# Kernel tuning notes

Measured on AMD Instinct MI355X. Metric: run time of the kernel, lower is better.

Reference implementation:

```python
import jax, jax.numpy as jnp
import numpy as np

N_NODES = 100000
N_EDGES = 1000000
D_FEAT = 64


def setup_inputs() -> dict:
    key = jax.random.key(0)
    k1, k2 = jax.random.split(key)
    x = jax.random.normal(k1, (N_NODES, D_FEAT), dtype=jnp.float32)
    edge_index = jax.random.randint(k2, (2, N_EDGES), 0, N_NODES, dtype=jnp.int64)
    return {"x": x, "edge_index": edge_index}


def reference(x, edge_index):
    # message: x_j = x[edge_index[1]]  (per-edge gather)
    # aggregate: scatter_add into destination nodes edge_index[0], dim_size = N
    # update: identity
    msg = x[edge_index[1]]                                  # [E, d]
    out = jax.ops.segment_sum(msg, edge_index[0], num_segments=x.shape[0])  # [N, d]
    return out
```

## Files before the change

### kernel.cpp

```cpp
#include <hip/hip_runtime.h>

#define D_FEAT     64
#define CSHIFT     8
#define CNODES     256
#define MAXC       512
#define CCAP       3072
#define CNT_STRIDE 16
#define PACK_SHIFT 24
#define PSRC_MASK  ((1 << PACK_SHIFT) - 1)
#define P_BLOCK    512
#define P_EPT      8
#define PB_EDGES   (P_BLOCK * P_EPT)
#define A_BLOCK    512
#define QCAP       1024

__global__ __launch_bounds__(256) void mp_scatter_kernel(
    const float* __restrict__ x,
    const int* __restrict__ ei,
    float* __restrict__ out,
    int E) {
    long long tid = (long long)blockIdx.x * blockDim.x + threadIdx.x;
    int e = (int)(tid >> 6);
    int f = (int)(tid & 63);
    if (e >= E) return;
    int dst = ei[e];
    int src = ei[E + e];
    float v = x[(long long)src * D_FEAT + f];
    unsafeAtomicAdd(&out[(long long)dst * D_FEAT + f], v);
}

__global__ __launch_bounds__(P_BLOCK) void partition_edges(
    const int* __restrict__ ei, int E, int nbins,
    int* __restrict__ binCount,
    int* __restrict__ binList) {
    __shared__ int  hist[MAXC];
    __shared__ int  loff[MAXC];
    __shared__ int  gbase[MAXC];
    __shared__ int  cur[MAXC];
    __shared__ int2 sOut[PB_EDGES];

    int t = threadIdx.x;
    for (int b = t; b < nbins; b += P_BLOCK) hist[b] = 0;
    __syncthreads();

    int start = blockIdx.x * PB_EDGES;
    int ecnt = E - start; if (ecnt > PB_EDGES) ecnt = PB_EDGES;

#pragma unroll
    for (int k = 0; k < P_EPT; ++k) {
        int i = k * P_BLOCK + t;
        if (i < ecnt) atomicAdd(&hist[ei[start + i] >> CSHIFT], 1);
    }
    __syncthreads();

    if (t < 64) {
        int chunk = (nbins + 63) >> 6;
        int base_i = t * chunk;
        int vals[8];
        int sum = 0;
        for (int k = 0; k < chunk; ++k) {
            int b = base_i + k;
            vals[k] = (b < nbins) ? hist[b] : 0;
            sum += vals[k];
        }
        int inc = sum;
#pragma unroll
        for (int d = 1; d < 64; d <<= 1) {
            int y = __shfl_up(inc, d, 64);
            if (t >= d) inc += y;
        }
        int excl = inc - sum;
        for (int k = 0; k < chunk; ++k) {
            int b = base_i + k;
            if (b < nbins) { loff[b] = excl; cur[b] = excl; excl += vals[k]; }
        }
    }
    __syncthreads();

    for (int b = t; b < nbins; b += P_BLOCK) {
        int h = hist[b];
        if (h) gbase[b] = atomicAdd(&binCount[b * CNT_STRIDE], h);
    }
    __syncthreads();

#pragma unroll
    for (int k = 0; k < P_EPT; ++k) {
        int i = k * P_BLOCK + t;
        if (i < ecnt) {
            int dst = ei[start + i];
            int src = ei[E + start + i];
            int b = dst >> CSHIFT;
            int r = atomicAdd(&cur[b], 1);
            int gpos = gbase[b] + (r - loff[b]);
            int slot = (gpos < CCAP) ? (b * CCAP + gpos) : -1;
            sOut[r] = make_int2(slot,
                                (int)(((unsigned)(dst & (CNODES - 1)) << PACK_SHIFT) |
                                      (unsigned)src));
        }
    }
    __syncthreads();

    for (int i = t; i < ecnt; i += P_BLOCK) {
        int2 o = sOut[i];
        if (o.x >= 0) binList[o.x] = o.y;
    }
}

__global__ __launch_bounds__(A_BLOCK, 8) void bin_accumulate(
    const float* __restrict__ x,
    const int* __restrict__ binCount,
    const int* __restrict__ binList,
    float* __restrict__ out,
    int N) {
    __shared__ int sList[CCAP];
    __shared__ int sCsr[QCAP];
    __shared__ int sCnt[64];
    __shared__ int sOff[64];
    __shared__ int sRank[64];

    int coarse  = blockIdx.x >> 2;
    int quarter = blockIdx.x & 3;
    int t = threadIdx.x;

    int cnt = binCount[coarse * CNT_STRIDE];
    if (cnt > CCAP) cnt = CCAP;

    if (t < 64) sCnt[t] = 0;
    __syncthreads();

    for (int i = t; i < cnt; i += A_BLOCK) {
        int p = binList[coarse * CCAP + i];
        sList[i] = p;
        unsigned ld = ((unsigned)p) >> PACK_SHIFT;
        if ((int)(ld >> 6) == quarter) atomicAdd(&sCnt[ld & 63], 1);
    }
    __syncthreads();

    if (t < 64) {
        int c = sCnt[t];
        int inc = c;
#pragma unroll
        for (int d = 1; d < 64; d <<= 1) {
            int y = __shfl_up(inc, d, 64);
            if (t >= d) inc += y;
        }
        sOff[t] = inc - c;
        sRank[t] = inc - c;
    }
    __syncthreads();

    for (int i = t; i < cnt; i += A_BLOCK) {
        int p = sList[i];
        unsigned ld = ((unsigned)p) >> PACK_SHIFT;
        if ((int)(ld >> 6) == quarter) {
            int r = atomicAdd(&sRank[ld & 63], 1);
            if (r < QCAP) sCsr[r] = p & PSRC_MASK;
        }
    }
    __syncthreads();

    int wave = t >> 6;
    int lane = t & 63;
    int q    = lane >> 4;
    int sub  = lane & 15;

    int nodeBase = (coarse << CSHIFT) + (quarter << 6);
    int nodesInQ = N - nodeBase; if (nodesInQ > 64) nodesInQ = 64;

    for (int n = wave; n < nodesInQ; n += 8) {
        int off = sOff[n];
        int deg = sCnt[n];
        if (off + deg > QCAP) deg = (QCAP > off) ? (QCAP - off) : 0;
        float4 acc = make_float4(0.f, 0.f, 0.f, 0.f);

        for (int e0 = 0; e0 < deg; e0 += 16) {
            float4 v[4];
#pragma unroll
            for (int j = 0; j < 4; ++j) {
                int eidx = e0 + j * 4 + q;
                v[j] = make_float4(0.f, 0.f, 0.f, 0.f);
                if (eidx < deg) {
                    int s = sCsr[off + eidx];
                    v[j] = ((const float4*)(x + (long long)s * D_FEAT))[sub];
                }
            }
#pragma unroll
            for (int j = 0; j < 4; ++j) {
                acc.x += v[j].x; acc.y += v[j].y;
                acc.z += v[j].z; acc.w += v[j].w;
            }
        }

        acc.x += __shfl_xor(acc.x, 16, 64);
        acc.y += __shfl_xor(acc.y, 16, 64);
        acc.z += __shfl_xor(acc.z, 16, 64);
        acc.w += __shfl_xor(acc.w, 16, 64);
        acc.x += __shfl_xor(acc.x, 32, 64);
        acc.y += __shfl_xor(acc.y, 32, 64);
        acc.z += __shfl_xor(acc.z, 32, 64);
        acc.w += __shfl_xor(acc.w, 32, 64);

        if (q == 0) {
            float4* out4 = (float4*)(out + (long long)(nodeBase + n) * D_FEAT);
            out4[sub] = acc;
        }
    }
}

extern "C" void kernel_launch(void* const* d_in, const int* in_sizes, int n_in,
                              void* d_out, int out_size, void* d_ws, size_t ws_size,
                              hipStream_t stream) {
    const float* x   = (const float*)d_in[0];
    const int*   ei  = (const int*)d_in[1];
    float*       out = (float*)d_out;

    int E = in_sizes[1] / 2;
    int N = out_size / D_FEAT;
    int nbins = (N + CNODES - 1) >> CSHIFT;

    size_t list_bytes  = (size_t)nbins * CCAP * sizeof(int);
    size_t count_bytes = (size_t)nbins * CNT_STRIDE * sizeof(int);
    size_t need = list_bytes + count_bytes;

    if (nbins > MAXC || N > (1 << PACK_SHIFT) || ws_size < need) {
        hipMemsetAsync(out, 0, (size_t)out_size * sizeof(float), stream);
        long long total = (long long)E * D_FEAT;
        int block = 256;
        int grid = (int)((total + block - 1) / block);
        mp_scatter_kernel<<<grid, block, 0, stream>>>(x, ei, out, E);
        return;
    }

    int* binList  = (int*)d_ws;
    int* binCount = (int*)((char*)d_ws + list_bytes);

    hipMemsetAsync(binCount, 0, count_bytes, stream);

    {
        int grid = (E + PB_EDGES - 1) / PB_EDGES;
        partition_edges<<<grid, P_BLOCK, 0, stream>>>(ei, E, nbins, binCount, binList);
    }
    {
        bin_accumulate<<<nbins * 4, A_BLOCK, 0, stream>>>(x, binCount, binList, out, N);
    }
}
```

Baseline: 128.0 us.

## Vectorize edge loads, halve accumulate blocks, and process two nodes per wave

The partition kernel now loads four contiguous edges per thread as int4 into registers, with half the edges per block, so the index array is read once instead of twice. The accumulate kernel splits each coarse bin into halves of 128 nodes instead of quarters of 64, which cuts the redundant rereads of binList per bin. It copies the bin list with int4 loads and has each wave interleave the gathers for two nodes so more loads are in flight. The cost is more registers, a lower occupancy hint, and work wasted when the two interleaved nodes have unequal degrees.

```diff
diff --git a/kernel.cpp b/kernel.cpp
--- a/kernel.cpp
+++ b/kernel.cpp
@@ -9,10 +9,10 @@
 #define PACK_SHIFT 24
 #define PSRC_MASK  ((1 << PACK_SHIFT) - 1)
 #define P_BLOCK    512
-#define P_EPT      8
+#define P_EPT      4
 #define PB_EDGES   (P_BLOCK * P_EPT)
 #define A_BLOCK    512
-#define QCAP       1024
+#define HCAP       2048
 
 __global__ __launch_bounds__(256) void mp_scatter_kernel(
     const float* __restrict__ x,
@@ -41,15 +41,31 @@
 
     int t = threadIdx.x;
     for (int b = t; b < nbins; b += P_BLOCK) hist[b] = 0;
-    __syncthreads();
 
     int start = blockIdx.x * PB_EDGES;
     int ecnt = E - start; if (ecnt > PB_EDGES) ecnt = PB_EDGES;
 
+    int dk[P_EPT], sk[P_EPT];
+    bool vec = (ecnt == PB_EDGES) && ((E & 3) == 0);
+    if (vec) {
+        int4 d4 = ((const int4*)(ei + start))[t];
+        int4 s4 = ((const int4*)(ei + E + start))[t];
+        dk[0] = d4.x; dk[1] = d4.y; dk[2] = d4.z; dk[3] = d4.w;
+        sk[0] = s4.x; sk[1] = s4.y; sk[2] = s4.z; sk[3] = s4.w;
+    } else {
+#pragma unroll
+        for (int k = 0; k < P_EPT; ++k) {
+            int i = t * P_EPT + k;
+            dk[k] = (i < ecnt) ? ei[start + i] : 0;
+            sk[k] = (i < ecnt) ? ei[E + start + i] : 0;
+        }
+    }
+    __syncthreads();
+
 #pragma unroll
     for (int k = 0; k < P_EPT; ++k) {
-        int i = k * P_BLOCK + t;
-        if (i < ecnt) atomicAdd(&hist[ei[start + i] >> CSHIFT], 1);
+        int i = t * P_EPT + k;
+        if (i < ecnt) atomicAdd(&hist[dk[k] >> CSHIFT], 1);
     }
     __syncthreads();
 
@@ -85,17 +101,16 @@
 
 #pragma unroll
     for (int k = 0; k < P_EPT; ++k) {
-        int i = k * P_BLOCK + t;
+        int i = t * P_EPT + k;
         if (i < ecnt) {
-            int dst = ei[start + i];
-            int src = ei[E + start + i];
+            int dst = dk[k];
             int b = dst >> CSHIFT;
             int r = atomicAdd(&cur[b], 1);
             int gpos = gbase[b] + (r - loff[b]);
             int slot = (gpos < CCAP) ? (b * CCAP + gpos) : -1;
             sOut[r] = make_int2(slot,
                                 (int)(((unsigned)(dst & (CNODES - 1)) << PACK_SHIFT) |
-                                      (unsigned)src));
+                                      (unsigned)sk[k]));
         }
     }
     __syncthreads();
@@ -106,55 +121,67 @@
     }
 }
 
-__global__ __launch_bounds__(A_BLOCK, 8) void bin_accumulate(
+__global__ __launch_bounds__(A_BLOCK, 6) void bin_accumulate(
     const float* __restrict__ x,
     const int* __restrict__ binCount,
     const int* __restrict__ binList,
     float* __restrict__ out,
     int N) {
     __shared__ int sList[CCAP];
-    __shared__ int sCsr[QCAP];
-    __shared__ int sCnt[64];
-    __shared__ int sOff[64];
-    __shared__ int sRank[64];
-
-    int coarse  = blockIdx.x >> 2;
-    int quarter = blockIdx.x & 3;
+    __shared__ int sCsr[HCAP];
+    __shared__ int sCnt[128];
+    __shared__ int sOff[128];
+    __shared__ int sRank[128];
+
+    int coarse = blockIdx.x >> 1;
+    int half   = blockIdx.x & 1;
     int t = threadIdx.x;
 
     int cnt = binCount[coarse * CNT_STRIDE];
     if (cnt > CCAP) cnt = CCAP;
 
-    if (t < 64) sCnt[t] = 0;
-    __syncthreads();
-
-    for (int i = t; i < cnt; i += A_BLOCK) {
-        int p = binList[coarse * CCAP + i];
-        sList[i] = p;
-        unsigned ld = ((unsigned)p) >> PACK_SHIFT;
-        if ((int)(ld >> 6) == quarter) atomicAdd(&sCnt[ld & 63], 1);
+    if (t < 128) sCnt[t] = 0;
+    __syncthreads();
+
+    const int4* bl4 = (const int4*)(binList + coarse * CCAP);
+    int nvec = (cnt + 3) >> 2;
+    for (int v = t; v < nvec; v += A_BLOCK) {
+        int4 e4 = bl4[v];
+        ((int4*)sList)[v] = e4;
+        int pk[4] = {e4.x, e4.y, e4.z, e4.w};
+        int i = v << 2;
+#pragma unroll
+        for (int j = 0; j < 4; ++j) {
+            if (i + j < cnt) {
+                unsigned ld = ((unsigned)pk[j]) >> PACK_SHIFT;
+                if ((int)(ld >> 7) == half) atomicAdd(&sCnt[ld & 127], 1);
+            }
+        }
     }
     __syncthreads();
 
     if (t < 64) {
-        int c = sCnt[t];
-        int inc = c;
+        int c0 = sCnt[2 * t];
+        int c1 = sCnt[2 * t + 1];
+        int sum = c0 + c1;
+        int inc = sum;
 #pragma unroll
         for (int d = 1; d < 64; d <<= 1) {
             int y = __shfl_up(inc, d, 64);
             if (t >= d) inc += y;
         }
-        sOff[t] = inc - c;
-        sRank[t] = inc - c;
+        int excl = inc - sum;
+        sOff[2 * t]     = excl;      sRank[2 * t]     = excl;
+        sOff[2 * t + 1] = excl + c0; sRank[2 * t + 1] = excl + c0;
     }
     __syncthreads();
 
     for (int i = t; i < cnt; i += A_BLOCK) {
         int p = sList[i];
         unsigned ld = ((unsigned)p) >> PACK_SHIFT;
-        if ((int)(ld >> 6) == quarter) {
-            int r = atomicAdd(&sRank[ld & 63], 1);
-            if (r < QCAP) sCsr[r] = p & PSRC_MASK;
+        if ((int)(ld >> 7) == half) {
+            int r = atomicAdd(&sRank[ld & 127], 1);
+            if (r < HCAP) sCsr[r] = p & PSRC_MASK;
         }
     }
     __syncthreads();
@@ -164,45 +191,78 @@
     int q    = lane >> 4;
     int sub  = lane & 15;
 
-    int nodeBase = (coarse << CSHIFT) + (quarter << 6);
-    int nodesInQ = N - nodeBase; if (nodesInQ > 64) nodesInQ = 64;
-
-    for (int n = wave; n < nodesInQ; n += 8) {
-        int off = sOff[n];
-        int deg = sCnt[n];
-        if (off + deg > QCAP) deg = (QCAP > off) ? (QCAP - off) : 0;
-        float4 acc = make_float4(0.f, 0.f, 0.f, 0.f);
-
-        for (int e0 = 0; e0 < deg; e0 += 16) {
-            float4 v[4];
+    int nodeBase = (coarse << CSHIFT) + (half << 7);
+    int nodesInH = N - nodeBase; if (nodesInH > 128) nodesInH = 128;
+
+    for (int n0 = wave; n0 < nodesInH; n0 += 16) {
+        int n1 = n0 + 8;
+        int hasB = (n1 < nodesInH);
+
+        int offA = sOff[n0];
+        int degA = sCnt[n0];
+        if (offA + degA > HCAP) degA = (HCAP > offA) ? (HCAP - offA) : 0;
+        int offB = 0, degB = 0;
+        if (hasB) {
+            offB = sOff[n1];
+            degB = sCnt[n1];
+            if (offB + degB > HCAP) degB = (HCAP > offB) ? (HCAP - offB) : 0;
+        }
+
+        float4 accA = make_float4(0.f, 0.f, 0.f, 0.f);
+        float4 accB = make_float4(0.f, 0.f, 0.f, 0.f);
+        int dmax = degA > degB ? degA : degB;
+
+        for (int e0 = 0; e0 < dmax; e0 += 16) {
+            float4 vA[4], vB[4];
 #pragma unroll
             for (int j = 0; j < 4; ++j) {
                 int eidx = e0 + j * 4 + q;
-                v[j] = make_float4(0.f, 0.f, 0.f, 0.f);
-                if (eidx < deg) {
-                    int s = sCsr[off + eidx];
-                    v[j] = ((const float4*)(x + (long long)s * D_FEAT))[sub];
+                vA[j] = make_float4(0.f, 0.f, 0.f, 0.f);
+                if (eidx < degA) {
+                    int s = sCsr[offA + eidx];
+                    vA[j] = ((const float4*)(x + (long long)s * D_FEAT))[sub];
                 }
             }
 #pragma unroll
             for (int j = 0; j < 4; ++j) {
-                acc.x += v[j].x; acc.y += v[j].y;
-                acc.z += v[j].z; acc.w += v[j].w;
+                int eidx = e0 + j * 4 + q;
+                vB[j] = make_float4(0.f, 0.f, 0.f, 0.f);
+                if (eidx < degB) {
+                    int s = sCsr[offB + eidx];
+                    vB[j] = ((const float4*)(x + (long long)s * D_FEAT))[sub];
+                }
             }
-        }
-
-        acc.x += __shfl_xor(acc.x, 16, 64);
-        acc.y += __shfl_xor(acc.y, 16, 64);
-        acc.z += __shfl_xor(acc.z, 16, 64);
-        acc.w += __shfl_xor(acc.w, 16, 64);
-        acc.x += __shfl_xor(acc.x, 32, 64);
-        acc.y += __shfl_xor(acc.y, 32, 64);
-        acc.z += __shfl_xor(acc.z, 32, 64);
-        acc.w += __shfl_xor(acc.w, 32, 64);
+#pragma unroll
+            for (int j = 0; j < 4; ++j) {
+                accA.x += vA[j].x; accA.y += vA[j].y;
+                accA.z += vA[j].z; accA.w += vA[j].w;
+                accB.x += vB[j].x; accB.y += vB[j].y;
+                accB.z += vB[j].z; accB.w += vB[j].w;
+            }
+        }
+
+        accA.x += __shfl_xor(accA.x, 16, 64);
+        accA.y += __shfl_xor(accA.y, 16, 64);
+        accA.z += __shfl_xor(accA.z, 16, 64);
+        accA.w += __shfl_xor(accA.w, 16, 64);
+        accA.x += __shfl_xor(accA.x, 32, 64);
+        accA.y += __shfl_xor(accA.y, 32, 64);
+        accA.z += __shfl_xor(accA.z, 32, 64);
+        accA.w += __shfl_xor(accA.w, 32, 64);
+
+        accB.x += __shfl_xor(accB.x, 16, 64);
+        accB.y += __shfl_xor(accB.y, 16, 64);
+        accB.z += __shfl_xor(accB.z, 16, 64);
+        accB.w += __shfl_xor(accB.w, 16, 64);
+        accB.x += __shfl_xor(accB.x, 32, 64);
+        accB.y += __shfl_xor(accB.y, 32, 64);
+        accB.z += __shfl_xor(accB.z, 32, 64);
+        accB.w += __shfl_xor(accB.w, 32, 64);
 
         if (q == 0) {
-            float4* out4 = (float4*)(out + (long long)(nodeBase + n) * D_FEAT);
-            out4[sub] = acc;
+            ((float4*)(out + (long long)(nodeBase + n0) * D_FEAT))[sub] = accA;
+            if (hasB)
+                ((float4*)(out + (long long)(nodeBase + n1) * D_FEAT))[sub] = accB;
         }
     }
 }
@@ -241,6 +301,6 @@
         partition_edges<<<grid, P_BLOCK, 0, stream>>>(ei, E, nbins, binCount, binList);
     }
     {
-        bin_accumulate<<<nbins * 4, A_BLOCK, 0, stream>>>(x, binCount, binList, out, N);
+        bin_accumulate<<<nbins * 2, A_BLOCK, 0, stream>>>(x, binCount, binList, out, N);
     }
 }
```

New measurement: 133.2 us. +4.0%, slower.
